# Kernel tuning notes

Measured on AMD Instinct MI355X. Metric: run time of the kernel, lower is better.

Reference implementation:

```python
import jax, jax.numpy as jnp
import numpy as np

N = 100000      # nodes
F_IN = 256      # num_node_features
E = 1600000     # edges (before self-loops)
DIMS = [F_IN, 128, 100, 32, 2]  # GCNConv layer widths


def _glorot(key, fan_in, fan_out):
    s = jnp.sqrt(6.0 / (fan_in + fan_out))
    return jax.random.uniform(key, (fan_in, fan_out), jnp.float32, -s, s)


def setup_inputs() -> dict:
    key = jax.random.key(0)
    ks = jax.random.split(key, 10)
    x = jax.random.normal(ks[0], (N, F_IN), jnp.float32)
    edge_index = jax.random.randint(ks[1], (2, E), 0, N, jnp.int32)
    inp = {"x": x, "edge_index": edge_index}
    for i in range(4):
        inp[f"W{i+1}"] = _glorot(ks[2 + 2 * i], DIMS[i], DIMS[i + 1])
        inp[f"b{i+1}"] = jnp.zeros((DIMS[i + 1],), jnp.float32)
    return inp


def reference(x, edge_index, W1, b1, W2, b2, W3, b3, W4, b4):
    n = x.shape[0]
    loops = jnp.arange(n, dtype=edge_index.dtype)
    src = jnp.concatenate([edge_index[0], loops])  # [E+N]
    dst = jnp.concatenate([edge_index[1], loops])
    # symmetric normalization: deg^-1/2[src] * deg^-1/2[dst] (self-loops included)
    deg = jax.ops.segment_sum(jnp.ones_like(src, x.dtype), dst, num_segments=n)
    dis = jax.lax.rsqrt(jnp.maximum(deg, 1.0))
    norm = (dis[src] * dis[dst])[:, None]  # [E+N, 1]

    def conv(h, W, b):
        h = h @ W                                      # [N, out]
        msg = h[src] * norm                            # gather + scale [E+N, out]
        return jax.ops.segment_sum(msg, dst, num_segments=n) + b

    h = jax.nn.leaky_relu(conv(x, W1, b1), negative_slope=0.1)
    h = jax.nn.leaky_relu(conv(h, W2, b2), negative_slope=0.1)
    h = jax.nn.leaky_relu(conv(h, W3, b3), negative_slope=0.1)
    h = conv(h, W4, b4)
    return jax.nn.softmax(h, axis=-1)
```

## Files before the change

kernel.cpp:

```cpp
#include <hip/hip_runtime.h>
#include <math.h>


typedef unsigned short ushort_t;
typedef unsigned int   uint_t;
typedef short  bf16x8 __attribute__((ext_vector_type(8)));
typedef float  f32x4  __attribute__((ext_vector_type(4)));

#define BKT_SHIFT 8
#define BKT_CAP   5120
#define BIN_CHUNK 4096

__device__ __forceinline__ ushort_t f2bf(float f) {
    union { float f; uint_t u; } v; v.f = f;
    uint_t u = v.u;
    u += 0x7fffu + ((u >> 16) & 1u);
    return (ushort_t)(u >> 16);
}
__device__ __forceinline__ float bflo(uint_t u) {
    union { uint_t q; float f; } v; v.q = u << 16; return v.f;
}
__device__ __forceinline__ float bfhi(uint_t u) {
    union { uint_t q; float f; } v; v.q = u & 0xffff0000u; return v.f;
}


__global__ __launch_bounds__(256) void bin_kernel(const int* __restrict__ srcArr,
                                                  const int* __restrict__ dstArr,
                                                  int* __restrict__ bkt_cursor,
                                                  uint2* __restrict__ staging,
                                                  int E, int nb) {
    __shared__ int hist[512];
    __shared__ int base[512];
    for (int b = threadIdx.x; b < 512; b += 256) hist[b] = 0;
    __syncthreads();
    const int e0 = blockIdx.x * BIN_CHUNK;
    #pragma unroll 4
    for (int k = 0; k < BIN_CHUNK / 256; ++k) {
        int e = e0 + k * 256 + threadIdx.x;
        if (e < E) atomicAdd(&hist[dstArr[e] >> BKT_SHIFT], 1);
    }
    __syncthreads();
    for (int b = threadIdx.x; b < nb; b += 256) {
        int h = hist[b];
        base[b] = h ? atomicAdd(&bkt_cursor[b], h) : 0;
    }
    __syncthreads();
    for (int b = threadIdx.x; b < 512; b += 256) hist[b] = 0;
    __syncthreads();
    #pragma unroll 4
    for (int k = 0; k < BIN_CHUNK / 256; ++k) {
        int e = e0 + k * 256 + threadIdx.x;
        if (e < E) {
            int s = srcArr[e], d = dstArr[e];
            int b = d >> BKT_SHIFT;
            int p = atomicAdd(&hist[b], 1);
            int idx = base[b] + p;
            if (idx < BKT_CAP)
                staging[(size_t)b * BKT_CAP + idx] = make_uint2((uint_t)s, (uint_t)d);
        }
    }
}

__global__ __launch_bounds__(256) void deg_from_staging_kernel(const uint2* __restrict__ staging,
                                                               const int* __restrict__ bkt_cursor,
                                                               int* __restrict__ degi,
                                                               float* __restrict__ dis, int n) {
    __shared__ int cur[256];
    const int b  = blockIdx.x;
    const int lo = b << BKT_SHIFT;
    const int nl = min(256, n - lo);
    cur[threadIdx.x] = 0;
    __syncthreads();
    int cnt = min(bkt_cursor[b], BKT_CAP);
    for (int e = threadIdx.x; e < cnt; e += 256) {
        uint2 p = staging[(size_t)b * BKT_CAP + e];
        atomicAdd(&cur[(int)p.y - lo], 1);
    }
    __syncthreads();
    if ((int)threadIdx.x < nl) {
        int d = cur[threadIdx.x];
        degi[lo + threadIdx.x] = d;
        dis[lo + threadIdx.x] = rsqrtf((float)(d + 1));
    }
}

__global__ void scan_block_kernel(const int* __restrict__ degi, int* __restrict__ row_excl,
                                  int* __restrict__ bsums, int n) {
    __shared__ int buf[1024];
    int i = blockIdx.x * 1024 + threadIdx.x;
    int v = (i < n) ? degi[i] : 0;
    buf[threadIdx.x] = v;
    __syncthreads();
    for (int off = 1; off < 1024; off <<= 1) {
        int t = (threadIdx.x >= (unsigned)off) ? buf[threadIdx.x - off] : 0;
        __syncthreads();
        buf[threadIdx.x] += t;
        __syncthreads();
    }
    if (i < n) row_excl[i] = buf[threadIdx.x] - v;
    if (threadIdx.x == 1023) bsums[blockIdx.x] = buf[1023];
}

__global__ void scan_sums_kernel(int* __restrict__ bsums, int nb) {
    __shared__ int buf[128];
    int v = ((int)threadIdx.x < nb) ? bsums[threadIdx.x] : 0;
    buf[threadIdx.x] = v;
    __syncthreads();
    for (int off = 1; off < 128; off <<= 1) {
        int t = (threadIdx.x >= (unsigned)off) ? buf[threadIdx.x - off] : 0;
        __syncthreads();
        buf[threadIdx.x] += t;
        __syncthreads();
    }
    if ((int)threadIdx.x < nb) bsums[threadIdx.x] = buf[threadIdx.x] - v;
    if (threadIdx.x == 0) bsums[nb] = buf[127];
}

__global__ void scan_add_kernel(int* __restrict__ row_start, const int* __restrict__ bsums,
                                int n, int nb) {
    int i = blockIdx.x * blockDim.x + threadIdx.x;
    if (i < n) row_start[i] += bsums[i >> 10];
    else if (i == n) row_start[n] = bsums[nb];
}

__global__ __launch_bounds__(256) void csr_build_kernel(const uint2* __restrict__ staging,
                                                        const int* __restrict__ bkt_cursor,
                                                        const int* __restrict__ row_start,
                                                        int* __restrict__ csr_src, int n) {
    __shared__ int rs[257];
    __shared__ int cur[256];
    __shared__ int seg[BKT_CAP];
    const int b  = blockIdx.x;
    const int lo = b << BKT_SHIFT;
    const int nl = min(256, n - lo);
    if ((int)threadIdx.x <= nl) rs[threadIdx.x] = row_start[lo + threadIdx.x];
    cur[threadIdx.x] = 0;
    __syncthreads();
    const int sbase = rs[0];
    int cnt = min(bkt_cursor[b], BKT_CAP);
    for (int e = threadIdx.x; e < cnt; e += 256) {
        uint2 p = staging[(size_t)b * BKT_CAP + e];
        int ln = (int)p.y - lo;
        int q  = atomicAdd(&cur[ln], 1);
        seg[(rs[ln] - sbase) + q] = (int)p.x;
    }
    __syncthreads();
    for (int i = threadIdx.x; i < cnt; i += 256) csr_src[sbase + i] = seg[i];
}

__global__ void wt_all_kernel(const float* __restrict__ W1, const float* __restrict__ W2,
                              const float* __restrict__ W3,
                              ushort_t* __restrict__ Wt1, ushort_t* __restrict__ Wt2,
                              ushort_t* __restrict__ Wt3) {
    int idx = blockIdx.x * blockDim.x + threadIdx.x;
    if (idx < 32768) {
        int nn = idx >> 8, k = idx & 255;
        Wt1[idx] = f2bf(W1[(size_t)k * 128 + nn]);
    } else if (idx < 49152) {
        int j = idx - 32768;
        int nn = j >> 7, k = j & 127;
        float v = (nn < 100) ? W2[(size_t)k * 100 + nn] : 0.f;
        Wt2[j] = f2bf(v);
    } else if (idx < 57344) {
        int j = idx - 49152;
        int nn = j >> 7, k = j & 127;
        float v = (k < 100 && nn < 32) ? W3[(size_t)k * 32 + nn] : 0.f;
        Wt3[j] = f2bf(v);
    }
}

template <bool A_FP32, int NFR, int KFR>
__global__ __launch_bounds__(256, 2) void gemm_persist(const void* __restrict__ Av,
                                                       const ushort_t* __restrict__ Bt,
                                                       ushort_t* __restrict__ C,
                                                       const float* __restrict__ dis,
                                                       int M, int lda, int ldb, int ldc) {
    const int lane = threadIdx.x & 63;
    const int rsel = lane & 15;
    const int kq   = (lane >> 4) * 8;
    const int nOff = blockIdx.y * (NFR * 16);

    bf16x8 bfr[NFR][KFR];
    #pragma unroll
    for (int ni = 0; ni < NFR; ++ni)
        #pragma unroll
        for (int kf = 0; kf < KFR; ++kf)
            bfr[ni][kf] = *(const bf16x8*)(Bt + (size_t)(nOff + ni * 16 + rsel) * ldb
                                              + kf * 32 + kq);

    const int nSlab   = (M + 31) >> 5;
    const int wstride = gridDim.x * 4;
    for (int s = blockIdx.x * 4 + (threadIdx.x >> 6); s < nSlab; s += wstride) {
        const int row0 = s * 32;

        bf16x8 af[2][KFR];
        #pragma unroll
        for (int mi = 0; mi < 2; ++mi) {
            const int gm = row0 + mi * 16 + rsel;
            #pragma unroll
            for (int kf = 0; kf < KFR; ++kf) {
                bf16x8 v = {0, 0, 0, 0, 0, 0, 0, 0};
                if (gm < M) {
                    if (A_FP32) {
                        const float* A = (const float*)Av;
                        const float4 f0 = *(const float4*)(A + (size_t)gm * lda + kf * 32 + kq);
                        const float4 f1 = *(const float4*)(A + (size_t)gm * lda + kf * 32 + kq + 4);
                        ushort_t o[8] = { f2bf(f0.x), f2bf(f0.y), f2bf(f0.z), f2bf(f0.w),
                                          f2bf(f1.x), f2bf(f1.y), f2bf(f1.z), f2bf(f1.w) };
                        v = *(const bf16x8*)o;
                    } else {
                        const ushort_t* A = (const ushort_t*)Av;
                        v = *(const bf16x8*)(A + (size_t)gm * lda + kf * 32 + kq);
                    }
                }
                af[mi][kf] = v;
            }
        }

        f32x4 acc[2][NFR];
        #pragma unroll
        for (int mi = 0; mi < 2; ++mi)
            #pragma unroll
            for (int ni = 0; ni < NFR; ++ni) acc[mi][ni] = (f32x4){0.f, 0.f, 0.f, 0.f};

        #pragma unroll
        for (int kf = 0; kf < KFR; ++kf)
            #pragma unroll
            for (int mi = 0; mi < 2; ++mi)
                #pragma unroll
                for (int ni = 0; ni < NFR; ++ni)
                    acc[mi][ni] = __builtin_amdgcn_mfma_f32_16x16x32_bf16(
                        bfr[ni][kf], af[mi][kf], acc[mi][ni], 0, 0, 0);

        #pragma unroll
        for (int mi = 0; mi < 2; ++mi) {
            const int gm = row0 + mi * 16 + rsel;
            if (gm >= M) continue;
            const float d = dis[gm];
            #pragma unroll
            for (int ni = 0; ni < NFR; ++ni) {
                uint2 o;
                o.x = (uint_t)f2bf(acc[mi][ni][0] * d) | ((uint_t)f2bf(acc[mi][ni][1] * d) << 16);
                o.y = (uint_t)f2bf(acc[mi][ni][2] * d) | ((uint_t)f2bf(acc[mi][ni][3] * d) << 16);
                *(uint2*)(C + (size_t)gm * ldc + nOff + ni * 16 + (lane >> 4) * 4) = o;
            }
        }
    }
}

template <int F>
__global__ void aggregate128_kernel(const ushort_t* __restrict__ h, const int* __restrict__ row_start,
                                    const int* __restrict__ csr_src,
                                    const float* __restrict__ dis, const float* __restrict__ bias,
                                    ushort_t* __restrict__ out, int n) {
    int wid  = threadIdx.x >> 6;
    int lane = threadIdx.x & 63;
    int node = blockIdx.x * 4 + wid;
    if (node >= n) return;
    const int q  = lane >> 4;
    const int fb = (lane & 15) * 8;
    float a[8];
    #pragma unroll
    for (int j = 0; j < 8; ++j) a[j] = 0.f;

    int i = row_start[node], end = row_start[node + 1];

#define ACC8(U)                                                     \
    do {                                                            \
        a[0] += bflo((U).x); a[1] += bfhi((U).x);                   \
        a[2] += bflo((U).y); a[3] += bfhi((U).y);                   \
        a[4] += bflo((U).z); a[5] += bfhi((U).z);                   \
        a[6] += bflo((U).w); a[7] += bfhi((U).w);                   \
    } while (0)

    #pragma unroll 2
    for (; i + 8 <= end; i += 8) {
        int sA = csr_src[i + q];
        int sB = csr_src[i + 4 + q];
        uint4 u = *(const uint4*)(h + (size_t)sA * 128 + fb);
        uint4 v = *(const uint4*)(h + (size_t)sB * 128 + fb);
        ACC8(u);
        ACC8(v);
    }
    int r = end - i;
    if (r > 0) {
        if (q < r) {
            int sA = csr_src[i + q];
            uint4 u = *(const uint4*)(h + (size_t)sA * 128 + fb);
            ACC8(u);
        }
        if (q + 4 < r) {
            int sB = csr_src[i + 4 + q];
            uint4 v = *(const uint4*)(h + (size_t)sB * 128 + fb);
            ACC8(v);
        }
    }
#undef ACC8

    #pragma unroll
    for (int j = 0; j < 8; ++j) {
        a[j] += __shfl_xor(a[j], 16);
        a[j] += __shfl_xor(a[j], 32);
    }

    if (q == 0) {
        uint4 su = *(const uint4*)(h + (size_t)node * 128 + fb);
        a[0] += bflo(su.x); a[1] += bfhi(su.x);
        a[2] += bflo(su.y); a[3] += bfhi(su.y);
        a[4] += bflo(su.z); a[5] += bfhi(su.z);
        a[6] += bflo(su.w); a[7] += bfhi(su.w);
        float dn = dis[node];
        #pragma unroll
        for (int j = 0; j < 8; ++j) {
            float b = (fb + j < F) ? bias[fb + j] : 0.f;
            float v = a[j] * dn + b;
            v = (v > 0.f) ? v : 0.1f * v;
            if (fb + j >= F) v = 0.f;
            a[j] = v;
        }
        uint4 o;
        o.x = (uint_t)f2bf(a[0]) | ((uint_t)f2bf(a[1]) << 16);
        o.y = (uint_t)f2bf(a[2]) | ((uint_t)f2bf(a[3]) << 16);
        o.z = (uint_t)f2bf(a[4]) | ((uint_t)f2bf(a[5]) << 16);
        o.w = (uint_t)f2bf(a[6]) | ((uint_t)f2bf(a[7]) << 16);
        *(uint4*)(out + (size_t)node * 128 + fb) = o;
    }
}

__global__ void aggregate32_kernel(const ushort_t* __restrict__ h, const int* __restrict__ row_start,
                                   const int* __restrict__ csr_src,
                                   const float* __restrict__ dis, const float* __restrict__ bias,
                                   ushort_t* __restrict__ out, int n) {
    int lane16 = threadIdx.x & 15;
    int node = blockIdx.x * (blockDim.x >> 4) + (threadIdx.x >> 4);
    if (node >= n) return;
    const int f0 = 2 * lane16;
    uint_t v = *(const uint_t*)(h + (size_t)node * 32 + f0);
    float acc0 = bflo(v);
    float acc1 = bfhi(v);
    int i = row_start[node], end = row_start[node + 1];
    for (; i + 4 <= end; i += 4) {
        int s0 = csr_src[i], s1 = csr_src[i + 1], s2 = csr_src[i + 2], s3 = csr_src[i + 3];
        uint_t u0 = *(const uint_t*)(h + (size_t)s0 * 32 + f0);
        uint_t u1 = *(const uint_t*)(h + (size_t)s1 * 32 + f0);
        uint_t u2 = *(const uint_t*)(h + (size_t)s2 * 32 + f0);
        uint_t u3 = *(const uint_t*)(h + (size_t)s3 * 32 + f0);
        acc0 += bflo(u0) + bflo(u1) + bflo(u2) + bflo(u3);
        acc1 += bfhi(u0) + bfhi(u1) + bfhi(u2) + bfhi(u3);
    }
    for (; i < end; ++i) {
        int s = csr_src[i];
        uint_t u = *(const uint_t*)(h + (size_t)s * 32 + f0);
        acc0 += bflo(u); acc1 += bfhi(u);
    }
    float dn = dis[node];
    acc0 = acc0 * dn + bias[f0];
    acc1 = acc1 * dn + bias[f0 + 1];
    acc0 = (acc0 > 0.f) ? acc0 : 0.1f * acc0;
    acc1 = (acc1 > 0.f) ? acc1 : 0.1f * acc1;
    uint_t o = (uint_t)f2bf(acc0) | ((uint_t)f2bf(acc1) << 16);
    *(uint_t*)(out + (size_t)node * 32 + f0) = o;
}

__global__ void gemm32x2_kernel(const ushort_t* __restrict__ H, const float* __restrict__ W4,
                                const float* __restrict__ dis, float* __restrict__ C, int n) {
    int node = blockIdx.x * blockDim.x + threadIdx.x;
    if (node >= n) return;
    const uint_t* row = (const uint_t*)(H + (size_t)node * 32);
    float a0 = 0.f, a1 = 0.f;
    #pragma unroll
    for (int k2 = 0; k2 < 16; ++k2) {
        uint_t u = row[k2];
        float x0 = bflo(u), x1 = bfhi(u);
        int k = 2 * k2;
        a0 += x0 * W4[k * 2]     + x1 * W4[(k + 1) * 2];
        a1 += x0 * W4[k * 2 + 1] + x1 * W4[(k + 1) * 2 + 1];
    }
    float d = dis[node];
    C[2 * (size_t)node]     = a0 * d;
    C[2 * (size_t)node + 1] = a1 * d;
}

__global__ void aggregate2_softmax_kernel(const float* __restrict__ h, const int* __restrict__ row_start,
                                          const int* __restrict__ csr_src,
                                          const float* __restrict__ dis, const float* __restrict__ bias,
                                          float* __restrict__ out, int n) {
    int node = blockIdx.x * blockDim.x + threadIdx.x;
    if (node >= n) return;
    float a0 = h[2 * (size_t)node];
    float a1 = h[2 * (size_t)node + 1];
    int beg = row_start[node], end = row_start[node + 1];
    for (int i = beg; i < end; ++i) {
        int s = csr_src[i];
        a0 += h[2 * (size_t)s];
        a1 += h[2 * (size_t)s + 1];
    }
    float dn = dis[node];
    a0 = a0 * dn + bias[0];
    a1 = a1 * dn + bias[1];
    float m  = fmaxf(a0, a1);
    float e0 = expf(a0 - m), e1 = expf(a1 - m);
    float inv = 1.f / (e0 + e1);
    out[2 * (size_t)node]     = e0 * inv;
    out[2 * (size_t)node + 1] = e1 * inv;
}


extern "C" void kernel_launch(void* const* d_in, const int* in_sizes, int n_in,
                              void* d_out, int out_size, void* d_ws, size_t ws_size,
                              hipStream_t stream) {
    const float* x  = (const float*)d_in[0];
    const int*   ei = (const int*)d_in[1];
    const float* W1 = (const float*)d_in[2];
    const float* b1 = (const float*)d_in[3];
    const float* W2 = (const float*)d_in[4];
    const float* b2 = (const float*)d_in[5];
    const float* W3 = (const float*)d_in[6];
    const float* b3 = (const float*)d_in[7];
    const float* W4 = (const float*)d_in[8];
    const float* b4 = (const float*)d_in[9];

    const int N = in_sizes[0] / 256;
    const int E = in_sizes[1] / 2;
    const int* srcA = ei;
    const int* dstA = ei + E;
    const int nbkt = (N + 255) >> BKT_SHIFT;

    char* ws = (char*)d_ws;
    size_t off = 0;
    auto alloc = [&](size_t bytes) {
        void* p = ws + off;
        off = (off + bytes + 255) & ~(size_t)255;
        return p;
    };
    int*      degi       = (int*)alloc((size_t)N * 4);
    float*    dis        = (float*)alloc((size_t)N * 4);
    int*      row_start  = (int*)alloc((size_t)(N + 1) * 4);
    int*      bsums      = (int*)alloc(512 * 4);
    int*      bkt_cursor = (int*)alloc((size_t)nbkt * 4);
    int*      csr_src    = (int*)alloc((size_t)E * 4);
    uint2*    staging    = (uint2*)alloc((size_t)nbkt * BKT_CAP * 8);
    ushort_t* bufA       = (ushort_t*)alloc((size_t)N * 128 * 2);
    ushort_t* bufB       = (ushort_t*)alloc((size_t)N * 128 * 2);
    float*    C4         = (float*)alloc((size_t)N * 2 * 4);
    ushort_t* Wt1        = (ushort_t*)alloc((size_t)128 * 256 * 2);
    ushort_t* Wt2        = (ushort_t*)alloc((size_t)128 * 128 * 2);
    ushort_t* Wt3        = (ushort_t*)alloc((size_t)64 * 128 * 2);
    (void)ws_size;

    hipMemsetAsync(bkt_cursor, 0, (size_t)nbkt * 4, stream);

    bin_kernel<<<(E + BIN_CHUNK - 1) / BIN_CHUNK, 256, 0, stream>>>(
        srcA, dstA, bkt_cursor, staging, E, nbkt);
    deg_from_staging_kernel<<<nbkt, 256, 0, stream>>>(staging, bkt_cursor, degi, dis, N);
    const int nb = (N + 1023) >> 10;
    scan_block_kernel<<<nb, 1024, 0, stream>>>(degi, row_start, bsums, N);
    scan_sums_kernel<<<1, 128, 0, stream>>>(bsums, nb);
    scan_add_kernel<<<(N + 256) / 256, 256, 0, stream>>>(row_start, bsums, N, nb);
    csr_build_kernel<<<nbkt, 256, 0, stream>>>(staging, bkt_cursor, row_start, csr_src, N);

    wt_all_kernel<<<(57344 + 255) / 256, 256, 0, stream>>>(W1, W2, W3, Wt1, Wt2, Wt3);

    const int PGRID = 512;
    const int aggBlocks128 = (N + 3) / 4;
    const int aggBlocks32  = (N + 15) / 16;

    gemm_persist<true, 4, 8><<<dim3(PGRID, 2), 256, 0, stream>>>(
        x, Wt1, bufA, dis, N, 256, 256, 128);
    aggregate128_kernel<128><<<aggBlocks128, 256, 0, stream>>>(
        bufA, row_start, csr_src, dis, b1, bufB, N);
    gemm_persist<false, 8, 4><<<dim3(PGRID, 1), 256, 0, stream>>>(
        bufB, Wt2, bufA, dis, N, 128, 128, 128);
    aggregate128_kernel<100><<<aggBlocks128, 256, 0, stream>>>(
        bufA, row_start, csr_src, dis, b2, bufB, N);
    gemm_persist<false, 2, 4><<<dim3(PGRID, 1), 256, 0, stream>>>(
        bufB, Wt3, bufA, dis, N, 128, 128, 32);
    aggregate32_kernel<<<aggBlocks32, 256, 0, stream>>>(
        bufA, row_start, csr_src, dis, b3, bufB, N);
    gemm32x2_kernel<<<(N + 255) / 256, 256, 0, stream>>>(bufB, W4, dis, C4, N);
    aggregate2_softmax_kernel<<<(N + 255) / 256, 256, 0, stream>>>(
        C4, row_start, csr_src, dis, b4, (float*)d_out, N);
}
```

Baseline: 324.1 us.

## Stage GEMM weight tiles in swizzled LDS instead of registers

The persistent GEMM kernels used to hold their whole B-weight fragment in registers. They now load it once per block into an XOR-swizzled shared-memory tile and read fragments from LDS inside the k-loop. The A fragments are loaded in halves when K is large, which lowers register pressure so launch bounds can rise to 4 blocks per CU. Grid shapes also change: layer 2 is split across two column blocks and layer 3 gets a larger grid. The cost is an LDS read per k-step and possible bank conflicts in place of register-resident weights.

```diff
diff --git a/kernel.cpp b/kernel.cpp
--- a/kernel.cpp
+++ b/kernel.cpp
@@ -171,52 +171,36 @@
 }
 
 template <bool A_FP32, int NFR, int KFR>
-__global__ __launch_bounds__(256, 2) void gemm_persist(const void* __restrict__ Av,
-                                                       const ushort_t* __restrict__ Bt,
-                                                       ushort_t* __restrict__ C,
-                                                       const float* __restrict__ dis,
-                                                       int M, int lda, int ldb, int ldc) {
+__global__ __launch_bounds__(256, 4) void gemm_ldsb(const void* __restrict__ Av,
+                                                    const ushort_t* __restrict__ Bt,
+                                                    ushort_t* __restrict__ C,
+                                                    const float* __restrict__ dis,
+                                                    int M, int lda, int ldb, int ldc) {
+    constexpr int BROWS = NFR * 16;
+    constexpr int BCOLS = KFR * 32;
+    constexpr int GR    = BCOLS / 8;
+    __shared__ __attribute__((aligned(16))) ushort_t Bs[BROWS][BCOLS];
+
     const int lane = threadIdx.x & 63;
     const int rsel = lane & 15;
-    const int kq   = (lane >> 4) * 8;
-    const int nOff = blockIdx.y * (NFR * 16);
-
-    bf16x8 bfr[NFR][KFR];
-    #pragma unroll
-    for (int ni = 0; ni < NFR; ++ni)
-        #pragma unroll
-        for (int kf = 0; kf < KFR; ++kf)
-            bfr[ni][kf] = *(const bf16x8*)(Bt + (size_t)(nOff + ni * 16 + rsel) * ldb
-                                              + kf * 32 + kq);
+    const int q    = lane >> 4;
+    const int kq   = q * 8;
+    const int nOff = blockIdx.y * BROWS;
+
+    for (int idx = threadIdx.x; idx < BROWS * GR; idx += 256) {
+        int r = idx / GR, g = idx - r * GR;
+        int gs = g ^ (r & 7);
+        *(bf16x8*)&Bs[r][gs * 8] = *(const bf16x8*)(Bt + (size_t)(nOff + r) * ldb + g * 8);
+    }
+    __syncthreads();
+
+    constexpr int KH    = (KFR > 4) ? 2 : 1;
+    constexpr int CHUNK = KFR / KH;
 
     const int nSlab   = (M + 31) >> 5;
     const int wstride = gridDim.x * 4;
     for (int s = blockIdx.x * 4 + (threadIdx.x >> 6); s < nSlab; s += wstride) {
         const int row0 = s * 32;
-
-        bf16x8 af[2][KFR];
-        #pragma unroll
-        for (int mi = 0; mi < 2; ++mi) {
-            const int gm = row0 + mi * 16 + rsel;
-            #pragma unroll
-            for (int kf = 0; kf < KFR; ++kf) {
-                bf16x8 v = {0, 0, 0, 0, 0, 0, 0, 0};
-                if (gm < M) {
-                    if (A_FP32) {
-                        const float* A = (const float*)Av;
-                        const float4 f0 = *(const float4*)(A + (size_t)gm * lda + kf * 32 + kq);
-                        const float4 f1 = *(const float4*)(A + (size_t)gm * lda + kf * 32 + kq + 4);
-                        ushort_t o[8] = { f2bf(f0.x), f2bf(f0.y), f2bf(f0.z), f2bf(f0.w),
-                                          f2bf(f1.x), f2bf(f1.y), f2bf(f1.z), f2bf(f1.w) };
-                        v = *(const bf16x8*)o;
-                    } else {
-                        const ushort_t* A = (const ushort_t*)Av;
-                        v = *(const bf16x8*)(A + (size_t)gm * lda + kf * 32 + kq);
-                    }
-                }
-                af[mi][kf] = v;
-            }
-        }
 
         f32x4 acc[2][NFR];
         #pragma unroll
@@ -225,13 +209,49 @@
             for (int ni = 0; ni < NFR; ++ni) acc[mi][ni] = (f32x4){0.f, 0.f, 0.f, 0.f};
 
         #pragma unroll
-        for (int kf = 0; kf < KFR; ++kf)
+        for (int kh = 0; kh < KH; ++kh) {
+            bf16x8 af[2][CHUNK];
             #pragma unroll
-            for (int mi = 0; mi < 2; ++mi)
+            for (int mi = 0; mi < 2; ++mi) {
+                const int gm = row0 + mi * 16 + rsel;
                 #pragma unroll
-                for (int ni = 0; ni < NFR; ++ni)
-                    acc[mi][ni] = __builtin_amdgcn_mfma_f32_16x16x32_bf16(
-                        bfr[ni][kf], af[mi][kf], acc[mi][ni], 0, 0, 0);
+                for (int kf = 0; kf < CHUNK; ++kf) {
+                    const int kc = (kh * CHUNK + kf) * 32 + kq;
+                    bf16x8 v = {0, 0, 0, 0, 0, 0, 0, 0};
+                    if (gm < M) {
+                        if (A_FP32) {
+                            const float* A = (const float*)Av;
+                            const float4 f0 = *(const float4*)(A + (size_t)gm * lda + kc);
+                            const float4 f1 = *(const float4*)(A + (size_t)gm * lda + kc + 4);
+                            ushort_t o[8] = { f2bf(f0.x), f2bf(f0.y), f2bf(f0.z), f2bf(f0.w),
+                                              f2bf(f1.x), f2bf(f1.y), f2bf(f1.z), f2bf(f1.w) };
+                            v = *(const bf16x8*)o;
+                        } else {
+                            const ushort_t* A = (const ushort_t*)Av;
+                            v = *(const bf16x8*)(A + (size_t)gm * lda + kc);
+                        }
+                    }
+                    af[mi][kf] = v;
+                }
+            }
+            #pragma unroll
+            for (int kf = 0; kf < CHUNK; ++kf) {
+                const int kk = kh * CHUNK + kf;
+                bf16x8 bfr[NFR];
+                #pragma unroll
+                for (int ni = 0; ni < NFR; ++ni) {
+                    const int r  = ni * 16 + rsel;
+                    const int gs = (kk * 4 + q) ^ (r & 7);
+                    bfr[ni] = *(const bf16x8*)&Bs[r][gs * 8];
+                }
+                #pragma unroll
+                for (int mi = 0; mi < 2; ++mi)
+                    #pragma unroll
+                    for (int ni = 0; ni < NFR; ++ni)
+                        acc[mi][ni] = __builtin_amdgcn_mfma_f32_16x16x32_bf16(
+                            bfr[ni], af[mi][kf], acc[mi][ni], 0, 0, 0);
+            }
+        }
 
         #pragma unroll
         for (int mi = 0; mi < 2; ++mi) {
@@ -243,7 +263,7 @@
                 uint2 o;
                 o.x = (uint_t)f2bf(acc[mi][ni][0] * d) | ((uint_t)f2bf(acc[mi][ni][1] * d) << 16);
                 o.y = (uint_t)f2bf(acc[mi][ni][2] * d) | ((uint_t)f2bf(acc[mi][ni][3] * d) << 16);
-                *(uint2*)(C + (size_t)gm * ldc + nOff + ni * 16 + (lane >> 4) * 4) = o;
+                *(uint2*)(C + (size_t)gm * ldc + nOff + ni * 16 + q * 4) = o;
             }
         }
     }
@@ -462,19 +482,18 @@
 
     wt_all_kernel<<<(57344 + 255) / 256, 256, 0, stream>>>(W1, W2, W3, Wt1, Wt2, Wt3);
 
-    const int PGRID = 512;
     const int aggBlocks128 = (N + 3) / 4;
     const int aggBlocks32  = (N + 15) / 16;
 
-    gemm_persist<true, 4, 8><<<dim3(PGRID, 2), 256, 0, stream>>>(
+    gemm_ldsb<true, 4, 8><<<dim3(512, 2), 256, 0, stream>>>(
         x, Wt1, bufA, dis, N, 256, 256, 128);
     aggregate128_kernel<128><<<aggBlocks128, 256, 0, stream>>>(
         bufA, row_start, csr_src, dis, b1, bufB, N);
-    gemm_persist<false, 8, 4><<<dim3(PGRID, 1), 256, 0, stream>>>(
+    gemm_ldsb<false, 4, 4><<<dim3(512, 2), 256, 0, stream>>>(
         bufB, Wt2, bufA, dis, N, 128, 128, 128);
     aggregate128_kernel<100><<<aggBlocks128, 256, 0, stream>>>(
         bufA, row_start, csr_src, dis, b2, bufB, N);
-    gemm_persist<false, 2, 4><<<dim3(PGRID, 1), 256, 0, stream>>>(
+    gemm_ldsb<false, 2, 4><<<dim3(1024, 1), 256, 0, stream>>>(
         bufB, Wt3, bufA, dis, N, 128, 128, 32);
     aggregate32_kernel<<<aggBlocks32, 256, 0, stream>>>(
         bufA, row_start, csr_src, dis, b3, bufB, N);
```

New measurement: 367.9 us. 13.5% more time.
